# Optimization experiments

Hardware: AMD Instinct MI355X
Metric: run time of the kernel (lower is better)

## Reference

```python
import jax, jax.numpy as jnp
import numpy as np

B, S, H = 64, 2048, 512


def setup_inputs() -> dict:
    key = jax.random.key(0)
    ks = jax.random.split(key, 11)
    sc = 1.0 / np.sqrt(H)
    return {
        "encoder_output": jax.random.normal(ks[0], (B, S, H), jnp.float32),
        "decoder_hidden": jax.random.normal(ks[1], (B, H), jnp.float32),
        "coverage": jax.random.uniform(ks[2], (B, S), jnp.float32),
        # params (torch Linear: y = x @ W.T + b); we store W already transposed as [in, out]
        "Wh": jax.random.normal(ks[3], (H, H), jnp.float32) * sc,
        "bh": jax.random.normal(ks[4], (H,), jnp.float32) * sc,
        "Ws": jax.random.normal(ks[5], (H, H), jnp.float32) * sc,
        "bs": jax.random.normal(ks[6], (H,), jnp.float32) * sc,
        "Wc": jax.random.normal(ks[7], (1, H), jnp.float32) * sc,  # Linear(1, H)
        "bc": jax.random.normal(ks[8], (H,), jnp.float32) * sc,
        "v_w": jax.random.normal(ks[9], (H,), jnp.float32) * sc,   # Linear(H, 1) weight
        "v_b": jax.random.normal(ks[10], (1,), jnp.float32) * sc,
    }


def reference(encoder_output, decoder_hidden, coverage, Wh, bh, Ws, bs, Wc, bc, v_w, v_b):
    # encoder_feature: [B,S,H]
    enc_f = jnp.einsum('bsh,hk->bsk', encoder_output, Wh) + bh
    # decoder_feature: [B,1,H]
    dec_f = (decoder_hidden @ Ws + bs)[:, None, :]
    # coverage_feature: [B,S,H] = cov[...,None] @ Wc(1,H) + bc
    cov_f = coverage[:, :, None] * Wc[0] + bc
    feat = jnp.tanh(enc_f + dec_f + cov_f)          # [B,S,H]
    e_t = jnp.einsum('bsh,h->bs', feat, v_w) + v_b[0]  # [B,S]
    a_t = jax.nn.softmax(e_t, axis=-1)
    sum_coverage = coverage + a_t
    return a_t, sum_coverage
```

## Files before the change

kernel.cpp:

```cpp
#include <hip/hip_runtime.h>
#include <math.h>


#define B_ 64
#define S_ 2048
#define H_ 512
#define M_ (B_ * S_)

#define RPB 128
#define BN 32
#define NPH 16
#define PHB 32768

typedef __attribute__((ext_vector_type(4))) float f32x4;
typedef __attribute__((ext_vector_type(8))) short s16x8;
typedef unsigned int u32;

__device__ __forceinline__ short f2bf(float f) {
    unsigned u = __float_as_uint(f);
    u += 0x7fffu + ((u >> 16) & 1u);
    return (short)(u >> 16);
}

__device__ __forceinline__ s16x8 cvt8(float4 a, float4 b) {
    s16x8 r;
    r[0] = f2bf(a.x); r[1] = f2bf(a.y); r[2] = f2bf(a.z); r[3] = f2bf(a.w);
    r[4] = f2bf(b.x); r[5] = f2bf(b.y); r[6] = f2bf(b.z); r[7] = f2bf(b.w);
    return r;
}

__device__ __forceinline__ float fast_tanh(float x) {
    return 1.0f - 2.0f / (__expf(2.0f * x) + 1.0f);
}

__device__ __forceinline__ void dma16(const void* g, void* s) {
    __builtin_amdgcn_global_load_lds(
        (const __attribute__((address_space(1))) u32*)g,
        (__attribute__((address_space(3))) u32*)s, 16, 0, 0);
}

__global__ __launch_bounds__(256) void transpose_cast(
    const float* __restrict__ Wh, short* __restrict__ Bimg) {
    __shared__ float tile[32][33];
    const int n0 = blockIdx.x * 32, k0 = blockIdx.y * 32;
    const int tx = threadIdx.x & 31, ty = threadIdx.x >> 5;
#pragma unroll
    for (int r = 0; r < 32; r += 8)
        tile[ty + r][tx] = Wh[(size_t)(k0 + ty + r) * H_ + n0 + tx];
    __syncthreads();
    const int kw = k0 >> 5;
    const int q = tx >> 3, j = tx & 7;
#pragma unroll
    for (int r = 0; r < 32; r += 8) {
        const int n = n0 + ty + r;
        const int ph = n >> 5, v = (n >> 4) & 1, mln = n & 15;
        const size_t idx = (size_t)ph * 16384 + (size_t)kw * 1024 + v * 512
                         + (q * 16 + mln) * 8 + j;
        Bimg[idx] = f2bf(tile[tx][ty + r]);
    }
}

__global__ __launch_bounds__(256) void dec_kernel(
    const float* __restrict__ dh, const float* __restrict__ Ws,
    const float* __restrict__ bs, const float* __restrict__ bh,
    const float* __restrict__ bc, float* __restrict__ D) {
    const int b = blockIdx.x;
    const int h = blockIdx.y * 256 + threadIdx.x;
    __shared__ float sdh[H_];
    sdh[threadIdx.x] = dh[b * H_ + threadIdx.x];
    sdh[threadIdx.x + 256] = dh[b * H_ + threadIdx.x + 256];
    __syncthreads();
    float acc = bs[h] + bh[h] + bc[h];
#pragma unroll 8
    for (int k = 0; k < H_; ++k)
        acc = fmaf(sdh[k], Ws[k * H_ + h], acc);
    D[b * H_ + h] = acc;
}

__global__ __launch_bounds__(512, 4) void gemm_fused(
    const float* __restrict__ A,
    const short* __restrict__ Bimg,
    const float* __restrict__ cover,
    const float* __restrict__ Wc,
    const float* __restrict__ vw,
    const float* __restrict__ D,
    float* __restrict__ e_t) {
    __shared__ __align__(16) short Bs[2][BN * H_];

    const int tid = threadIdx.x;
    const int w = tid >> 6;
    const int l = tid & 63;
    const int q = l >> 4;
    const int ml = l & 15;

    const int row_blk = blockIdx.x * RPB;
    const int b = row_blk >> 11;
    const int r0 = row_blk + w * 16;

    {
        const char* g = (const char*)Bimg + (size_t)(w * 4) * 1024 + l * 16;
        char* s = (char*)&Bs[0][0] + (w * 4) * 1024;
#pragma unroll
        for (int c = 0; c < 4; ++c) dma16(g + c * 1024, s + c * 1024);
    }

    s16x8 a[16];
    {
        const float* ap = A + (size_t)(r0 + ml) * H_ + q * 8;
#pragma unroll
        for (int kw = 0; kw < 16; ++kw) {
            float4 x = *(const float4*)(ap + kw * 32);
            float4 y = *(const float4*)(ap + kw * 32 + 4);
            a[kw] = cvt8(x, y);
        }
    }

    float cv[4];
#pragma unroll
    for (int r = 0; r < 4; ++r) cv[r] = cover[r0 + q * 4 + r];

    float ecur[4] = {0.0f, 0.0f, 0.0f, 0.0f};

    __syncthreads();

    for (int ph = 0; ph < NPH; ++ph) {
        const int cur = ph & 1;

        if (ph + 1 < NPH) {
            const char* g = (const char*)Bimg + (size_t)(ph + 1) * PHB
                          + (size_t)(w * 4) * 1024 + l * 16;
            char* s = (char*)&Bs[cur ^ 1][0] + (w * 4) * 1024;
#pragma unroll
            for (int c = 0; c < 4; ++c) dma16(g + c * 1024, s + c * 1024);
        }

        const int n0 = ph * BN + ml;
        const float wc0 = Wc[n0],          wc1 = Wc[n0 + 16];
        const float vv0 = vw[n0],          vv1 = vw[n0 + 16];
        const float dd0 = D[b * H_ + n0],  dd1 = D[b * H_ + n0 + 16];

        const short* bp = &Bs[cur][0];
        f32x4 acc0 = (f32x4)0.0f, acc1 = (f32x4)0.0f;
#pragma unroll
        for (int kw = 0; kw < 16; ++kw) {
            s16x8 b0 = *(const s16x8*)(bp + kw * 1024 + l * 8);
            s16x8 b1 = *(const s16x8*)(bp + kw * 1024 + 512 + l * 8);
            acc0 = __builtin_amdgcn_mfma_f32_16x16x32_bf16(a[kw], b0, acc0, 0, 0, 0);
            acc1 = __builtin_amdgcn_mfma_f32_16x16x32_bf16(a[kw], b1, acc1, 0, 0, 0);
        }

#pragma unroll
        for (int r = 0; r < 4; ++r) {
            ecur[r] += vv0 * fast_tanh(acc0[r] + fmaf(cv[r], wc0, dd0));
            ecur[r] += vv1 * fast_tanh(acc1[r] + fmaf(cv[r], wc1, dd1));
        }

        __syncthreads();
    }

    float p0 = ecur[0], p1 = ecur[1], p2 = ecur[2], p3 = ecur[3];
#pragma unroll
    for (int s = 1; s < 16; s <<= 1) {
        p0 += __shfl_xor(p0, s, 64);
        p1 += __shfl_xor(p1, s, 64);
        p2 += __shfl_xor(p2, s, 64);
        p3 += __shfl_xor(p3, s, 64);
    }
    if (ml == 0) {
        float4 st = {p0, p1, p2, p3};
        *(float4*)&e_t[r0 + q * 4] = st;
    }
}

__global__ __launch_bounds__(256) void softmax_kernel(
    const float* __restrict__ e_t, const float* __restrict__ cover,
    const float* __restrict__ vb, float* __restrict__ out) {
    const int b = blockIdx.x;
    const int tid = threadIdx.x;
    const float vbv = vb[0];

    float e[8];
    float mx = -1e30f;
#pragma unroll
    for (int r = 0; r < 8; ++r) {
        e[r] = e_t[b * S_ + r * 256 + tid] + vbv;
        mx = fmaxf(mx, e[r]);
    }
#pragma unroll
    for (int off = 32; off >= 1; off >>= 1) mx = fmaxf(mx, __shfl_xor(mx, off, 64));

    __shared__ float sm[4], ss[4], sbc[2];
    const int wid = tid >> 6, lane = tid & 63;
    if (lane == 0) sm[wid] = mx;
    __syncthreads();
    if (tid == 0) sbc[0] = fmaxf(fmaxf(sm[0], sm[1]), fmaxf(sm[2], sm[3]));
    __syncthreads();
    mx = sbc[0];

    float ex[8];
    float sum = 0.0f;
#pragma unroll
    for (int r = 0; r < 8; ++r) {
        ex[r] = __expf(e[r] - mx);
        sum += ex[r];
    }
#pragma unroll
    for (int off = 32; off >= 1; off >>= 1) sum += __shfl_xor(sum, off, 64);
    if (lane == 0) ss[wid] = sum;
    __syncthreads();
    if (tid == 0) sbc[1] = ss[0] + ss[1] + ss[2] + ss[3];
    __syncthreads();
    const float inv = 1.0f / sbc[1];

#pragma unroll
    for (int r = 0; r < 8; ++r) {
        const int s = r * 256 + tid;
        const float a = ex[r] * inv;
        out[b * S_ + s] = a;
        out[M_ + b * S_ + s] = cover[b * S_ + s] + a;
    }
}

extern "C" void kernel_launch(void* const* d_in, const int* in_sizes, int n_in,
                              void* d_out, int out_size, void* d_ws, size_t ws_size,
                              hipStream_t stream) {
    const float* enc = (const float*)d_in[0];
    const float* dh  = (const float*)d_in[1];
    const float* cov = (const float*)d_in[2];
    const float* Wh  = (const float*)d_in[3];
    const float* bh  = (const float*)d_in[4];
    const float* Ws  = (const float*)d_in[5];
    const float* bs  = (const float*)d_in[6];
    const float* Wc  = (const float*)d_in[7];
    const float* bc  = (const float*)d_in[8];
    const float* vw  = (const float*)d_in[9];
    const float* vb  = (const float*)d_in[10];
    float* out = (float*)d_out;

    float* e_t  = (float*)d_ws;
    float* Dws  = e_t + M_;
    short* Whbt = (short*)(Dws + B_ * H_);

    transpose_cast<<<dim3(H_ / 32, H_ / 32), 256, 0, stream>>>(Wh, Whbt);
    dec_kernel<<<dim3(B_, 2), 256, 0, stream>>>(dh, Ws, bs, bh, bc, Dws);
    gemm_fused<<<M_ / RPB, 512, 0, stream>>>(enc, Whbt, cov, Wc, vw, Dws, e_t);
    softmax_kernel<<<B_, 256, 0, stream>>>(e_t, cov, vb, out);
}
```

Measured before the change: 499.8 us.

## Use 4-wave blocks with 32 rows per wave and triple-buffered B phases

Halves the block to 256 threads, so each wave now holds A fragments for 32 rows and reuses each LDS B fragment across two MFMAs instead of loading two B fragments per A. The B tile shrinks to 16 columns per phase with a three-deep LDS ring, prefetched two phases ahead. A single barrier per phase is gated by a partial vmcnt wait, replacing the double-buffer with two syncs. This is meant to cut LDS read traffic and barrier stalls. In exchange, register pressure rises from doubling the A fragments, and there are twice as many phases.

```diff
diff --git a/kernel.cpp b/kernel.cpp
--- a/kernel.cpp
+++ b/kernel.cpp
@@ -8,9 +8,10 @@
 #define M_ (B_ * S_)
 
 #define RPB 128
-#define BN 32
-#define NPH 16
-#define PHB 32768
+#define BN 16
+#define NPH 32
+#define PHS (BN * H_)
+#define PHBYTES (PHS * 2)
 
 typedef __attribute__((ext_vector_type(4))) float f32x4;
 typedef __attribute__((ext_vector_type(8))) short s16x8;
@@ -53,9 +54,9 @@
 #pragma unroll
     for (int r = 0; r < 32; r += 8) {
         const int n = n0 + ty + r;
-        const int ph = n >> 5, v = (n >> 4) & 1, mln = n & 15;
-        const size_t idx = (size_t)ph * 16384 + (size_t)kw * 1024 + v * 512
-                         + (q * 16 + mln) * 8 + j;
+        const int ph = n >> 4, mln = n & 15;
+        const size_t idx = (size_t)ph * PHS + (size_t)kw * 512
+                         + q * 128 + mln * 8 + j;
         Bimg[idx] = f2bf(tile[tx][ty + r]);
     }
 }
@@ -77,7 +78,7 @@
     D[b * H_ + h] = acc;
 }
 
-__global__ __launch_bounds__(512, 4) void gemm_fused(
+__global__ __launch_bounds__(256, 3) void gemm_fused(
     const float* __restrict__ A,
     const short* __restrict__ Bimg,
     const float* __restrict__ cover,
@@ -85,7 +86,7 @@
     const float* __restrict__ vw,
     const float* __restrict__ D,
     float* __restrict__ e_t) {
-    __shared__ __align__(16) short Bs[2][BN * H_];
+    __shared__ __align__(16) short Bs[3 * PHS];
 
     const int tid = threadIdx.x;
     const int w = tid >> 6;
@@ -95,80 +96,100 @@
 
     const int row_blk = blockIdx.x * RPB;
     const int b = row_blk >> 11;
-    const int r0 = row_blk + w * 16;
+    const int r0 = row_blk + w * 32;
+
+    const int chunk0 = w * 4;
 
     {
-        const char* g = (const char*)Bimg + (size_t)(w * 4) * 1024 + l * 16;
-        char* s = (char*)&Bs[0][0] + (w * 4) * 1024;
-#pragma unroll
-        for (int c = 0; c < 4; ++c) dma16(g + c * 1024, s + c * 1024);
-    }
-
-    s16x8 a[16];
+        const char* g0 = (const char*)Bimg + chunk0 * 1024 + l * 16;
+        char* s0 = (char*)Bs + chunk0 * 1024;
+#pragma unroll
+        for (int c = 0; c < 4; ++c) dma16(g0 + c * 1024, s0 + c * 1024);
+        const char* g1 = g0 + PHBYTES;
+        char* s1 = s0 + PHBYTES;
+#pragma unroll
+        for (int c = 0; c < 4; ++c) dma16(g1 + c * 1024, s1 + c * 1024);
+    }
+
+    s16x8 a[2][16];
     {
         const float* ap = A + (size_t)(r0 + ml) * H_ + q * 8;
 #pragma unroll
         for (int kw = 0; kw < 16; ++kw) {
-            float4 x = *(const float4*)(ap + kw * 32);
-            float4 y = *(const float4*)(ap + kw * 32 + 4);
-            a[kw] = cvt8(x, y);
-        }
-    }
-
-    float cv[4];
-#pragma unroll
-    for (int r = 0; r < 4; ++r) cv[r] = cover[r0 + q * 4 + r];
-
-    float ecur[4] = {0.0f, 0.0f, 0.0f, 0.0f};
-
-    __syncthreads();
-
-    for (int ph = 0; ph < NPH; ++ph) {
-        const int cur = ph & 1;
-
-        if (ph + 1 < NPH) {
-            const char* g = (const char*)Bimg + (size_t)(ph + 1) * PHB
-                          + (size_t)(w * 4) * 1024 + l * 16;
-            char* s = (char*)&Bs[cur ^ 1][0] + (w * 4) * 1024;
-#pragma unroll
-            for (int c = 0; c < 4; ++c) dma16(g + c * 1024, s + c * 1024);
-        }
-
-        const int n0 = ph * BN + ml;
-        const float wc0 = Wc[n0],          wc1 = Wc[n0 + 16];
-        const float vv0 = vw[n0],          vv1 = vw[n0 + 16];
-        const float dd0 = D[b * H_ + n0],  dd1 = D[b * H_ + n0 + 16];
-
-        const short* bp = &Bs[cur][0];
+#pragma unroll
+            for (int t = 0; t < 2; ++t) {
+                const float* p = ap + (size_t)t * 16 * H_ + kw * 32;
+                float4 x = *(const float4*)p;
+                float4 y = *(const float4*)(p + 4);
+                a[t][kw] = cvt8(x, y);
+            }
+        }
+    }
+
+    float cv[2][4];
+#pragma unroll
+    for (int t = 0; t < 2; ++t)
+#pragma unroll
+        for (int r = 0; r < 4; ++r)
+            cv[t][r] = cover[r0 + t * 16 + q * 4 + r];
+
+    float ecur[2][4] = {};
+
+    int cur = 0;
+    const char* gdma = (const char*)Bimg + 2 * (size_t)PHBYTES
+                     + chunk0 * 1024 + l * 16;
+
+    for (int p = 0; p < NPH; ++p) {
+        asm volatile("s_waitcnt vmcnt(4)" ::: "memory");
+        __builtin_amdgcn_sched_barrier(0);
+        __builtin_amdgcn_s_barrier();
+
+        const int n0 = p * BN + ml;
+        const float wc = Wc[n0];
+        const float vv = vw[n0];
+        const float dd = D[b * H_ + n0];
+        __builtin_amdgcn_sched_barrier(0);
+
+        if (p + 2 < NPH) {
+            const int nb = (cur == 0) ? 2 : cur - 1;
+            char* sd = (char*)Bs + nb * PHBYTES + chunk0 * 1024;
+#pragma unroll
+            for (int c = 0; c < 4; ++c) dma16(gdma + c * 1024, sd + c * 1024);
+            gdma += PHBYTES;
+        }
+
+        const short* bp = Bs + cur * PHS;
         f32x4 acc0 = (f32x4)0.0f, acc1 = (f32x4)0.0f;
 #pragma unroll
         for (int kw = 0; kw < 16; ++kw) {
-            s16x8 b0 = *(const s16x8*)(bp + kw * 1024 + l * 8);
-            s16x8 b1 = *(const s16x8*)(bp + kw * 1024 + 512 + l * 8);
-            acc0 = __builtin_amdgcn_mfma_f32_16x16x32_bf16(a[kw], b0, acc0, 0, 0, 0);
-            acc1 = __builtin_amdgcn_mfma_f32_16x16x32_bf16(a[kw], b1, acc1, 0, 0, 0);
+            s16x8 bfr = *(const s16x8*)(bp + kw * 512 + l * 8);
+            acc0 = __builtin_amdgcn_mfma_f32_16x16x32_bf16(a[0][kw], bfr, acc0, 0, 0, 0);
+            acc1 = __builtin_amdgcn_mfma_f32_16x16x32_bf16(a[1][kw], bfr, acc1, 0, 0, 0);
         }
 
 #pragma unroll
         for (int r = 0; r < 4; ++r) {
-            ecur[r] += vv0 * fast_tanh(acc0[r] + fmaf(cv[r], wc0, dd0));
-            ecur[r] += vv1 * fast_tanh(acc1[r] + fmaf(cv[r], wc1, dd1));
-        }
-
-        __syncthreads();
-    }
-
-    float p0 = ecur[0], p1 = ecur[1], p2 = ecur[2], p3 = ecur[3];
-#pragma unroll
-    for (int s = 1; s < 16; s <<= 1) {
-        p0 += __shfl_xor(p0, s, 64);
-        p1 += __shfl_xor(p1, s, 64);
-        p2 += __shfl_xor(p2, s, 64);
-        p3 += __shfl_xor(p3, s, 64);
-    }
-    if (ml == 0) {
-        float4 st = {p0, p1, p2, p3};
-        *(float4*)&e_t[r0 + q * 4] = st;
+            ecur[0][r] += vv * fast_tanh(acc0[r] + fmaf(cv[0][r], wc, dd));
+            ecur[1][r] += vv * fast_tanh(acc1[r] + fmaf(cv[1][r], wc, dd));
+        }
+
+        cur = (cur == 2) ? 0 : cur + 1;
+    }
+
+#pragma unroll
+    for (int t = 0; t < 2; ++t) {
+        float p0 = ecur[t][0], p1 = ecur[t][1], p2 = ecur[t][2], p3 = ecur[t][3];
+#pragma unroll
+        for (int s = 1; s < 16; s <<= 1) {
+            p0 += __shfl_xor(p0, s, 64);
+            p1 += __shfl_xor(p1, s, 64);
+            p2 += __shfl_xor(p2, s, 64);
+            p3 += __shfl_xor(p3, s, 64);
+        }
+        if (ml == 0) {
+            float4 st = {p0, p1, p2, p3};
+            *(float4*)&e_t[r0 + t * 16 + q * 4] = st;
+        }
     }
 }
 
@@ -243,6 +264,6 @@
 
     transpose_cast<<<dim3(H_ / 32, H_ / 32), 256, 0, stream>>>(Wh, Whbt);
     dec_kernel<<<dim3(B_, 2), 256, 0, stream>>>(dh, Ws, bs, bh, bc, Dws);
-    gemm_fused<<<M_ / RPB, 512, 0, stream>>>(enc, Whbt, cov, Wc, vw, Dws, e_t);
+    gemm_fused<<<M_ / RPB, 256, 0, stream>>>(enc, Whbt, cov, Wc, vw, Dws, e_t);
     softmax_kernel<<<B_, 256, 0, stream>>>(e_t, cov, vb, out);
 }
```

Result: slower. 573.4 us (+14.7%).
